# Optimization experiments

Hardware: AMD Instinct MI355X
Metric: run time of the kernel (lower is better)

## Reference

```python
import jax, jax.numpy as jnp
import numpy as np

B, R, C, NC = 8, 1000, 1024, 81
H, W = 1024, 1024
MEANS = jnp.array([0.0, 0.0, 0.0, 0.0], jnp.float32)
STDS = jnp.array([0.1, 0.1, 0.2, 0.2], jnp.float32)
MIN_CONF = 0.05
NMS_THR = 0.5
MAX_INST = 100
NEG = -1e9


def setup_inputs() -> dict:
    key = jax.random.key(0)
    k1, k2, k3, k4, k5 = jax.random.split(key, 5)
    x = jax.random.normal(k1, (B * R, C), jnp.float32)
    w_cls = jax.random.normal(k2, (C, NC), jnp.float32) * 0.01
    b_cls = jnp.zeros((NC,), jnp.float32)
    w_delta = jax.random.normal(k3, (C, 4), jnp.float32) * 0.01
    b_delta = jnp.zeros((4,), jnp.float32)
    # rois: (batch_ind, y1, x1, y2, x2), normalized coords with y1<y2, x1<x2
    yx1 = jax.random.uniform(k4, (B * R, 2), jnp.float32) * 0.7
    hw = jax.random.uniform(k5, (B * R, 2), jnp.float32) * 0.28 + 0.02
    bind = jnp.repeat(jnp.arange(B, dtype=jnp.float32), R)[:, None]
    rois = jnp.concatenate([bind, yx1, yx1 + hw], axis=1)
    return {"x": x, "w_cls": w_cls, "b_cls": b_cls, "w_delta": w_delta, "b_delta": b_delta, "rois": rois}


def delta2bbox(rois, deltas):
    # rois, deltas: [N, 4] in (y1, x1, y2, x2) / (dy, dx, dh, dw)
    d = deltas * STDS + MEANS
    h = rois[:, 2] - rois[:, 0]
    w = rois[:, 3] - rois[:, 1]
    cy = rois[:, 0] + 0.5 * h + d[:, 0] * h
    cx = rois[:, 1] + 0.5 * w + d[:, 1] * w
    h = h * jnp.exp(d[:, 2])
    w = w * jnp.exp(d[:, 3])
    return jnp.stack([cy - 0.5 * h, cx - 0.5 * w, cy + 0.5 * h, cx + 0.5 * w], axis=1)


def pairwise_iou(boxes):
    # boxes: [N, 4]
    area = (boxes[:, 2] - boxes[:, 0]) * (boxes[:, 3] - boxes[:, 1])
    y1 = jnp.maximum(boxes[:, None, 0], boxes[None, :, 0])
    x1 = jnp.maximum(boxes[:, None, 1], boxes[None, :, 1])
    y2 = jnp.minimum(boxes[:, None, 2], boxes[None, :, 2])
    x2 = jnp.minimum(boxes[:, None, 3], boxes[None, :, 3])
    inter = jnp.maximum(y2 - y1, 0.0) * jnp.maximum(x2 - x1, 0.0)
    union = area[:, None] + area[None, :] - inter
    return inter / jnp.maximum(union, 1e-8)


def nms_single(boxes, scores, class_ids, valid):
    # boxes [R,4], scores [R], class_ids [R] int, valid [R] bool -> detections [MAX_INST, 6]
    masked = jnp.where(valid, scores, NEG)
    order = jnp.argsort(-masked)  # descending score
    b = boxes[order]
    s = masked[order]
    c = class_ids[order]
    v = valid[order]
    # class-aware IoU: cross-class pairs never suppress each other
    iou = pairwise_iou(b) * (c[:, None] == c[None, :]).astype(boxes.dtype)
    n = b.shape[0]

    def step(supp, xs):
        i, iou_row, vi = xs
        keep_i = vi & ~supp[i]
        supp = supp | jnp.where(keep_i, iou_row > NMS_THR, False)
        return supp, keep_i

    _, keep = jax.lax.scan(step, jnp.zeros((n,), bool), (jnp.arange(n), iou, v))
    final = jnp.where(keep, s, NEG)
    top_s, top_i = jax.lax.top_k(final, MAX_INST)
    ok = (top_s > NEG / 2)[:, None]
    det = jnp.concatenate([b[top_i], c[top_i].astype(boxes.dtype)[:, None], s[top_i][:, None]], axis=1)
    return jnp.where(ok, det, 0.0)


def reference(x, w_cls, b_cls, w_delta, b_delta, rois):
    logits = x @ w_cls + b_cls                      # [B*R, NC]
    probs = jax.nn.softmax(logits, axis=-1)
    deltas = x @ w_delta + b_delta                  # [B*R, 4]

    probs_b = probs.reshape(B, R, NC)
    class_ids = jnp.argmax(probs_b, axis=-1).astype(jnp.int32)           # [B, R]
    class_scores = jnp.take_along_axis(probs_b, class_ids[..., None], axis=-1)[..., 0]

    scale = jnp.array([H, W, H, W], jnp.float32)
    boxes = rois[:, 1:5] * scale                    # pixel coords, [B*R, 4]
    refined = delta2bbox(boxes, deltas)
    window = jnp.array([0.0, 0.0, float(H), float(W)], jnp.float32)
    refined = jnp.clip(refined, window[jnp.array([0, 1, 0, 1])], window[jnp.array([2, 3, 2, 3])])
    refined = refined.reshape(B, R, 4)

    valid = (class_ids > 0) & (class_scores >= MIN_CONF)
    detections = jax.vmap(nms_single)(refined, class_scores, class_ids, valid)  # [B, MAX_INST, 6]
    return detections
```

## Files before the change

### kernel.cpp

```cpp
#include <hip/hip_runtime.h>
#include <math.h>
#include <stdint.h>

#define RR 1000
#define CC 1024
#define NCLS 81
#define HH 1024.0f
#define MIN_CONF_V 0.05f
#define NMS_THR_V 0.5f
#define NEGV -1e9f

typedef __attribute__((ext_vector_type(8))) short bf16x8;
typedef __attribute__((ext_vector_type(4))) float f32x4;

__device__ __forceinline__ unsigned short f2bf(float f) {
    unsigned int u = __float_as_uint(f);
    return (unsigned short)((u + 0x7FFFu + ((u >> 16) & 1u)) >> 16);
}
__device__ __forceinline__ float bf2f(unsigned short h) {
    return __uint_as_float(((unsigned int)h) << 16);
}

__global__ __launch_bounds__(64) void k0_pack(
    const float* __restrict__ w_cls, const float* __restrict__ w_delta,
    unsigned short* __restrict__ wh, unsigned short* __restrict__ wl)
{
    const int ct = blockIdx.x >> 5;
    const int sg = blockIdx.x & 31;
    const int l = threadIdx.x;
    const int col = ct * 16 + (l & 15);
    const int kbase = sg * 32 + (l >> 4) * 8;
    unsigned short h[8], lo[8];
    #pragma unroll
    for (int j = 0; j < 8; ++j) {
        const int k = kbase + j;
        float v = 0.f;
        if (col < NCLS)          v = w_cls[(size_t)k * NCLS + col];
        else if (col < NCLS + 4) v = w_delta[(size_t)k * 4 + (col - NCLS)];
        h[j] = f2bf(v);
        lo[j] = f2bf(v - bf2f(h[j]));
    }
    const size_t base = ((size_t)(ct * 32 + sg) * 64 + l) * 8;
    uint4 uh, ul;
    uh.x = (unsigned)h[0] | ((unsigned)h[1] << 16);
    uh.y = (unsigned)h[2] | ((unsigned)h[3] << 16);
    uh.z = (unsigned)h[4] | ((unsigned)h[5] << 16);
    uh.w = (unsigned)h[6] | ((unsigned)h[7] << 16);
    ul.x = (unsigned)lo[0] | ((unsigned)lo[1] << 16);
    ul.y = (unsigned)lo[2] | ((unsigned)lo[3] << 16);
    ul.z = (unsigned)lo[4] | ((unsigned)lo[5] << 16);
    ul.w = (unsigned)lo[6] | ((unsigned)lo[7] << 16);
    *(uint4*)&wh[base] = uh;
    *(uint4*)&wl[base] = ul;
}

__global__ __launch_bounds__(384) void k1_head(
    const float* __restrict__ x,
    const unsigned short* __restrict__ wh, const unsigned short* __restrict__ wl,
    const float* __restrict__ b_cls, const float* __restrict__ b_delta,
    const float* __restrict__ rois,
    float* __restrict__ bx_ws, float* __restrict__ sc_ws, float* __restrict__ cid_ws)
{
    __shared__ __align__(16) unsigned short xh[2][16][64];
    __shared__ __align__(16) unsigned short xl[2][16][64];
    __shared__ float outb[16 * 104];

    const int t = threadIdx.x;
    const int lane = t & 63;
    const int ct = t >> 6;
    const int row0 = blockIdx.x * 16;

    const int srow = t >> 4;
    const int sk4 = (t & 15) * 4;
    const size_t xsrc = (size_t)(row0 + srow) * CC + sk4;

    const int aoff0 = (lane & 15) * 64 + ((lane >> 4) << 3);
    const int aoff1 = aoff0 + 32;

    const unsigned short* whp = wh + ((size_t)(ct * 32) * 64 + lane) * 8;
    const unsigned short* wlp = wl + ((size_t)(ct * 32) * 64 + lane) * 8;
    const size_t bstep = 64 * 8;

    f32x4 acc = {0.f, 0.f, 0.f, 0.f};

    float4 xv = make_float4(0.f, 0.f, 0.f, 0.f);
    if (t < 256) xv = *(const float4*)(x + xsrc);

    bf16x8 B0h = *(const bf16x8*)(whp + 0 * bstep);
    bf16x8 B0l = *(const bf16x8*)(wlp + 0 * bstep);
    bf16x8 B1h = *(const bf16x8*)(whp + 1 * bstep);
    bf16x8 B1l = *(const bf16x8*)(wlp + 1 * bstep);

    int cur = 0;
    for (int c = 0; c < 16; ++c) {
        if (t < 256) {
            unsigned short h0 = f2bf(xv.x), h1 = f2bf(xv.y), h2 = f2bf(xv.z), h3 = f2bf(xv.w);
            ushort4 hv = make_ushort4(h0, h1, h2, h3);
            ushort4 lv = make_ushort4(f2bf(xv.x - bf2f(h0)), f2bf(xv.y - bf2f(h1)),
                                      f2bf(xv.z - bf2f(h2)), f2bf(xv.w - bf2f(h3)));
            *(ushort4*)&xh[cur][srow][sk4] = hv;
            *(ushort4*)&xl[cur][srow][sk4] = lv;
        }
        __syncthreads();

        bf16x8 N0h, N0l, N1h, N1l;
        if (c < 15) {
            if (t < 256) xv = *(const float4*)(x + xsrc + (size_t)(c + 1) * 64);
            const size_t sg = (size_t)(2 * c + 2);
            N0h = *(const bf16x8*)(whp + sg * bstep);
            N0l = *(const bf16x8*)(wlp + sg * bstep);
            N1h = *(const bf16x8*)(whp + (sg + 1) * bstep);
            N1l = *(const bf16x8*)(wlp + (sg + 1) * bstep);
        }

        const bf16x8 a0h = *(const bf16x8*)&((const unsigned short*)xh[cur])[aoff0];
        const bf16x8 a0l = *(const bf16x8*)&((const unsigned short*)xl[cur])[aoff0];
        acc = __builtin_amdgcn_mfma_f32_16x16x32_bf16(a0h, B0h, acc, 0, 0, 0);
        acc = __builtin_amdgcn_mfma_f32_16x16x32_bf16(a0h, B0l, acc, 0, 0, 0);
        acc = __builtin_amdgcn_mfma_f32_16x16x32_bf16(a0l, B0h, acc, 0, 0, 0);
        const bf16x8 a1h = *(const bf16x8*)&((const unsigned short*)xh[cur])[aoff1];
        const bf16x8 a1l = *(const bf16x8*)&((const unsigned short*)xl[cur])[aoff1];
        acc = __builtin_amdgcn_mfma_f32_16x16x32_bf16(a1h, B1h, acc, 0, 0, 0);
        acc = __builtin_amdgcn_mfma_f32_16x16x32_bf16(a1h, B1l, acc, 0, 0, 0);
        acc = __builtin_amdgcn_mfma_f32_16x16x32_bf16(a1l, B1h, acc, 0, 0, 0);

        B0h = N0h; B0l = N0l; B1h = N1h; B1l = N1l;
        cur ^= 1;
        __syncthreads();
    }

    #pragma unroll
    for (int r = 0; r < 4; ++r)
        outb[((lane >> 4) * 4 + r) * 104 + ct * 16 + (lane & 15)] = acc[r];
    __syncthreads();

    if (t < 256) {
        const int row = t >> 4;
        const int e = t & 15;
        float vmax = -INFINITY;
        int imax = 1 << 20;
        float v[6];
        #pragma unroll
        for (int s = 0; s < 6; ++s) {
            const int cidx = e + 16 * s;
            if (cidx < NCLS) {
                const float val = outb[row * 104 + cidx] + b_cls[cidx];
                v[s] = val;
                if (val > vmax) { vmax = val; imax = cidx; }
            } else v[s] = -INFINITY;
        }
        #pragma unroll
        for (int m = 8; m >= 1; m >>= 1) {
            const float v2 = __shfl_xor(vmax, m);
            const int   i2 = __shfl_xor(imax, m);
            if (v2 > vmax || (v2 == vmax && i2 < imax)) { vmax = v2; imax = i2; }
        }
        float sume = 0.f;
        #pragma unroll
        for (int s = 0; s < 6; ++s) {
            const int cidx = e + 16 * s;
            if (cidx < NCLS) sume += expf(v[s] - vmax);
        }
        #pragma unroll
        for (int m = 8; m >= 1; m >>= 1) sume += __shfl_xor(sume, m);

        if (e == 0) {
            const int gr = row0 + row;
            const float score = 1.0f / sume;
            const int cid = imax;
            const float d0 = (outb[row * 104 + 81] + b_delta[0]) * 0.1f;
            const float d1 = (outb[row * 104 + 82] + b_delta[1]) * 0.1f;
            const float d2 = (outb[row * 104 + 83] + b_delta[2]) * 0.2f;
            const float d3 = (outb[row * 104 + 84] + b_delta[3]) * 0.2f;
            const float y1 = rois[(size_t)gr * 5 + 1] * HH;
            const float x1 = rois[(size_t)gr * 5 + 2] * HH;
            const float y2 = rois[(size_t)gr * 5 + 3] * HH;
            const float x2 = rois[(size_t)gr * 5 + 4] * HH;
            const float h = y2 - y1, w = x2 - x1;
            const float cy = y1 + 0.5f * h + d0 * h;
            const float cx = x1 + 0.5f * w + d1 * w;
            const float h2 = h * expf(d2);
            const float w2 = w * expf(d3);
            const float by1 = fminf(fmaxf(cy - 0.5f * h2, 0.f), HH);
            const float bx1 = fminf(fmaxf(cx - 0.5f * w2, 0.f), HH);
            const float by2 = fminf(fmaxf(cy + 0.5f * h2, 0.f), HH);
            const float bx2 = fminf(fmaxf(cx + 0.5f * w2, 0.f), HH);
            const bool valid = (cid > 0) && (score >= MIN_CONF_V);
            bx_ws[(size_t)gr * 4 + 0] = by1;
            bx_ws[(size_t)gr * 4 + 1] = bx1;
            bx_ws[(size_t)gr * 4 + 2] = by2;
            bx_ws[(size_t)gr * 4 + 3] = bx2;
            sc_ws[gr]  = valid ? score : NEGV;
            cid_ws[gr] = (float)cid;
        }
    }
}

__global__ __launch_bounds__(256) void k2_nms(
    const float* __restrict__ bx_ws, const float* __restrict__ sc_ws,
    const float* __restrict__ cid_ws, float* __restrict__ det)
{
    __shared__ unsigned long long keys[256];
    __shared__ float sy1[256], sx1[256], sy2[256], sx2[256];
    __shared__ float scl[256], ssc[256];
    __shared__ unsigned char supp[256];
    __shared__ int s_cnt, s_num;

    const int b = blockIdx.x;
    const int t = threadIdx.x;
    const int base = b * RR;

    keys[t] = 0ull;
    if (t == 0) { s_cnt = 0; s_num = 0; }
    __syncthreads();

    for (int r = t; r < RR; r += 256) {
        const float s = sc_ws[base + r];
        if (s > NEGV * 0.5f) {
            const int i = atomicAdd(&s_num, 1);
            if (i < 256) {
                unsigned int u = __float_as_uint(s) | 0x80000000u;
                keys[i] = ((unsigned long long)u << 32) | (unsigned int)(~(unsigned int)r);
            }
        }
    }
    __syncthreads();
    const int V = (s_num < 256) ? s_num : 256;

    for (int k = 2; k <= 256; k <<= 1) {
        for (int j = k >> 1; j > 0; j >>= 1) {
            const int ixj = t ^ j;
            if (ixj > t) {
                const unsigned long long a = keys[t];
                const unsigned long long c = keys[ixj];
                const bool desc = ((t & k) == 0);
                if (desc ? (a < c) : (a > c)) { keys[t] = c; keys[ixj] = a; }
            }
            __syncthreads();
        }
    }

    if (t < V) {
        const int orig = (int)(~(unsigned int)keys[t]);
        const int g = base + orig;
        sy1[t] = bx_ws[(size_t)g * 4 + 0];
        sx1[t] = bx_ws[(size_t)g * 4 + 1];
        sy2[t] = bx_ws[(size_t)g * 4 + 2];
        sx2[t] = bx_ws[(size_t)g * 4 + 3];
        scl[t] = cid_ws[g];
        ssc[t] = sc_ws[g];
    } else {
        sy1[t] = sx1[t] = sy2[t] = sx2[t] = 0.f;
        scl[t] = -1.f;
        ssc[t] = NEGV;
    }
    supp[t] = 0;
    __syncthreads();

    for (int i = 0; i < V; ++i) {
        __syncthreads();
        if (s_cnt >= 100) break;
        if (!supp[i]) {
            if (t > i && t < V && scl[t] == scl[i]) {
                const float yy1 = fmaxf(sy1[i], sy1[t]);
                const float xx1 = fmaxf(sx1[i], sx1[t]);
                const float yy2 = fminf(sy2[i], sy2[t]);
                const float xx2 = fminf(sx2[i], sx2[t]);
                const float inter = fmaxf(yy2 - yy1, 0.f) * fmaxf(xx2 - xx1, 0.f);
                const float ai = (sy2[i] - sy1[i]) * (sx2[i] - sx1[i]);
                const float at = (sy2[t] - sy1[t]) * (sx2[t] - sx1[t]);
                const float uni = ai + at - inter;
                if (inter / fmaxf(uni, 1e-8f) > NMS_THR_V) supp[t] = 1;
            }
            if (t == 0) {
                const int slot = s_cnt;
                if (slot < 100) {
                    float* o = det + ((size_t)b * 100 + slot) * 6;
                    o[0] = sy1[i]; o[1] = sx1[i]; o[2] = sy2[i]; o[3] = sx2[i];
                    o[4] = scl[i]; o[5] = ssc[i];
                }
                s_cnt = slot + 1;
            }
        }
    }
    __syncthreads();
    int cnt = s_cnt;
    if (cnt > 100) cnt = 100;
    for (int idx = t; idx < 600; idx += 256) {
        if (idx >= cnt * 6) det[(size_t)b * 600 + idx] = 0.f;
    }
}

extern "C" void kernel_launch(void* const* d_in, const int* in_sizes, int n_in,
                              void* d_out, int out_size, void* d_ws, size_t ws_size,
                              hipStream_t stream) {
    const float* x       = (const float*)d_in[0];
    const float* w_cls   = (const float*)d_in[1];
    const float* b_cls   = (const float*)d_in[2];
    const float* w_delta = (const float*)d_in[3];
    const float* b_delta = (const float*)d_in[4];
    const float* rois    = (const float*)d_in[5];
    float* out = (float*)d_out;

    float* bx_ws   = (float*)d_ws;
    float* sc_ws   = bx_ws + 8000 * 4;
    float* cid_ws  = sc_ws + 8000;
    unsigned short* wh = (unsigned short*)(cid_ws + 8000);
    unsigned short* wl = wh + 98304;

    k0_pack<<<192, 64, 0, stream>>>(w_cls, w_delta, wh, wl);
    k1_head<<<500, 384, 0, stream>>>(x, wh, wl, b_cls, b_delta, rois,
                                     bx_ws, sc_ws, cid_ws);
    k2_nms<<<8, 256, 0, stream>>>(bx_ws, sc_ws, cid_ws, out);
}
```

Before: 32.99 us.

## Process 32 rows per head block and swizzle LDS to cut bank conflicts

The head GEMM block now covers 32 ROI rows instead of 16, so each wave runs two MFMA accumulator chains that share the same weight fragments. This halves the weight loads from global memory and halves the grid to 250 blocks. LDS staging of x uses an XOR swizzle on the column index to avoid bank conflicts on the fragment reads. The softmax epilogue is remapped to 8 lanes per row. In exchange there are fewer blocks than CUs to spread over, and per-thread work and register use go up.

Result: no change. 33.14 us (+0.4%).

```diff
diff --git a/kernel.cpp b/kernel.cpp
--- a/kernel.cpp
+++ b/kernel.cpp
@@ -61,30 +61,41 @@
     const float* __restrict__ rois,
     float* __restrict__ bx_ws, float* __restrict__ sc_ws, float* __restrict__ cid_ws)
 {
-    __shared__ __align__(16) unsigned short xh[2][16][64];
-    __shared__ __align__(16) unsigned short xl[2][16][64];
-    __shared__ float outb[16 * 104];
+    __shared__ __align__(16) unsigned short xh[2][32][64];
+    __shared__ __align__(16) unsigned short xl[2][32][64];
+    __shared__ float outb[32 * 104];
 
     const int t = threadIdx.x;
     const int lane = t & 63;
     const int ct = t >> 6;
-    const int row0 = blockIdx.x * 16;
-
-    const int srow = t >> 4;
-    const int sk4 = (t & 15) * 4;
-    const size_t xsrc = (size_t)(row0 + srow) * CC + sk4;
-
-    const int aoff0 = (lane & 15) * 64 + ((lane >> 4) << 3);
-    const int aoff1 = aoff0 + 32;
+    const int row0 = blockIdx.x * 32;
+
+    const int srow0 = t >> 4;
+    const int sc4 = t & 15;
+    const int sd0 = (sc4 ^ ((srow0 & 7) << 1)) * 4;
+    const size_t xsrc0 = (size_t)(row0 + srow0) * CC + sc4 * 4;
+    const int srow1 = 24 + (t >> 4);
+    const int sd1 = (sc4 ^ ((srow1 & 7) << 1)) * 4;
+    const size_t xsrc1 = (size_t)(row0 + srow1) * CC + sc4 * 4;
+
+    const int r = lane & 15;
+    const int m = lane >> 4;
+    const int e2 = (r & 7) << 1;
+    const int a00 = r * 64        + (((m << 1) + 0) ^ e2) * 4;
+    const int a01 = r * 64        + (((m << 1) + 8) ^ e2) * 4;
+    const int a10 = (r + 16) * 64 + (((m << 1) + 0) ^ e2) * 4;
+    const int a11 = (r + 16) * 64 + (((m << 1) + 8) ^ e2) * 4;
 
     const unsigned short* whp = wh + ((size_t)(ct * 32) * 64 + lane) * 8;
     const unsigned short* wlp = wl + ((size_t)(ct * 32) * 64 + lane) * 8;
     const size_t bstep = 64 * 8;
 
-    f32x4 acc = {0.f, 0.f, 0.f, 0.f};
-
-    float4 xv = make_float4(0.f, 0.f, 0.f, 0.f);
-    if (t < 256) xv = *(const float4*)(x + xsrc);
+    f32x4 acc0 = {0.f, 0.f, 0.f, 0.f};
+    f32x4 acc1 = {0.f, 0.f, 0.f, 0.f};
+
+    float4 xv0 = *(const float4*)(x + xsrc0);
+    float4 xv1 = make_float4(0.f, 0.f, 0.f, 0.f);
+    if (t < 128) xv1 = *(const float4*)(x + xsrc1);
 
     bf16x8 B0h = *(const bf16x8*)(whp + 0 * bstep);
     bf16x8 B0l = *(const bf16x8*)(wlp + 0 * bstep);
@@ -93,19 +104,27 @@
 
     int cur = 0;
     for (int c = 0; c < 16; ++c) {
-        if (t < 256) {
-            unsigned short h0 = f2bf(xv.x), h1 = f2bf(xv.y), h2 = f2bf(xv.z), h3 = f2bf(xv.w);
-            ushort4 hv = make_ushort4(h0, h1, h2, h3);
-            ushort4 lv = make_ushort4(f2bf(xv.x - bf2f(h0)), f2bf(xv.y - bf2f(h1)),
-                                      f2bf(xv.z - bf2f(h2)), f2bf(xv.w - bf2f(h3)));
-            *(ushort4*)&xh[cur][srow][sk4] = hv;
-            *(ushort4*)&xl[cur][srow][sk4] = lv;
+        {
+            unsigned short h0 = f2bf(xv0.x), h1 = f2bf(xv0.y), h2 = f2bf(xv0.z), h3 = f2bf(xv0.w);
+            *(ushort4*)&xh[cur][srow0][sd0] = make_ushort4(h0, h1, h2, h3);
+            *(ushort4*)&xl[cur][srow0][sd0] = make_ushort4(
+                f2bf(xv0.x - bf2f(h0)), f2bf(xv0.y - bf2f(h1)),
+                f2bf(xv0.z - bf2f(h2)), f2bf(xv0.w - bf2f(h3)));
+            if (t < 128) {
+                unsigned short g0 = f2bf(xv1.x), g1 = f2bf(xv1.y), g2 = f2bf(xv1.z), g3 = f2bf(xv1.w);
+                *(ushort4*)&xh[cur][srow1][sd1] = make_ushort4(g0, g1, g2, g3);
+                *(ushort4*)&xl[cur][srow1][sd1] = make_ushort4(
+                    f2bf(xv1.x - bf2f(g0)), f2bf(xv1.y - bf2f(g1)),
+                    f2bf(xv1.z - bf2f(g2)), f2bf(xv1.w - bf2f(g3)));
+            }
         }
         __syncthreads();
 
-        bf16x8 N0h, N0l, N1h, N1l;
+        bf16x8 N0h = B0h, N0l = B0l, N1h = B1h, N1l = B1l;
         if (c < 15) {
-            if (t < 256) xv = *(const float4*)(x + xsrc + (size_t)(c + 1) * 64);
+            const size_t off = (size_t)(c + 1) * 64;
+            xv0 = *(const float4*)(x + xsrc0 + off);
+            if (t < 128) xv1 = *(const float4*)(x + xsrc1 + off);
             const size_t sg = (size_t)(2 * c + 2);
             N0h = *(const bf16x8*)(whp + sg * bstep);
             N0l = *(const bf16x8*)(wlp + sg * bstep);
@@ -113,16 +132,28 @@
             N1l = *(const bf16x8*)(wlp + (sg + 1) * bstep);
         }
 
-        const bf16x8 a0h = *(const bf16x8*)&((const unsigned short*)xh[cur])[aoff0];
-        const bf16x8 a0l = *(const bf16x8*)&((const unsigned short*)xl[cur])[aoff0];
-        acc = __builtin_amdgcn_mfma_f32_16x16x32_bf16(a0h, B0h, acc, 0, 0, 0);
-        acc = __builtin_amdgcn_mfma_f32_16x16x32_bf16(a0h, B0l, acc, 0, 0, 0);
-        acc = __builtin_amdgcn_mfma_f32_16x16x32_bf16(a0l, B0h, acc, 0, 0, 0);
-        const bf16x8 a1h = *(const bf16x8*)&((const unsigned short*)xh[cur])[aoff1];
-        const bf16x8 a1l = *(const bf16x8*)&((const unsigned short*)xl[cur])[aoff1];
-        acc = __builtin_amdgcn_mfma_f32_16x16x32_bf16(a1h, B1h, acc, 0, 0, 0);
-        acc = __builtin_amdgcn_mfma_f32_16x16x32_bf16(a1h, B1l, acc, 0, 0, 0);
-        acc = __builtin_amdgcn_mfma_f32_16x16x32_bf16(a1l, B1h, acc, 0, 0, 0);
+        const unsigned short* hb = (const unsigned short*)xh[cur];
+        const unsigned short* lb = (const unsigned short*)xl[cur];
+        const bf16x8 a0h = *(const bf16x8*)(hb + a00);
+        const bf16x8 a0l = *(const bf16x8*)(lb + a00);
+        const bf16x8 a2h = *(const bf16x8*)(hb + a10);
+        const bf16x8 a2l = *(const bf16x8*)(lb + a10);
+        acc0 = __builtin_amdgcn_mfma_f32_16x16x32_bf16(a0h, B0h, acc0, 0, 0, 0);
+        acc1 = __builtin_amdgcn_mfma_f32_16x16x32_bf16(a2h, B0h, acc1, 0, 0, 0);
+        acc0 = __builtin_amdgcn_mfma_f32_16x16x32_bf16(a0h, B0l, acc0, 0, 0, 0);
+        acc1 = __builtin_amdgcn_mfma_f32_16x16x32_bf16(a2h, B0l, acc1, 0, 0, 0);
+        acc0 = __builtin_amdgcn_mfma_f32_16x16x32_bf16(a0l, B0h, acc0, 0, 0, 0);
+        acc1 = __builtin_amdgcn_mfma_f32_16x16x32_bf16(a2l, B0h, acc1, 0, 0, 0);
+        const bf16x8 a1h = *(const bf16x8*)(hb + a01);
+        const bf16x8 a1l = *(const bf16x8*)(lb + a01);
+        const bf16x8 a3h = *(const bf16x8*)(hb + a11);
+        const bf16x8 a3l = *(const bf16x8*)(lb + a11);
+        acc0 = __builtin_amdgcn_mfma_f32_16x16x32_bf16(a1h, B1h, acc0, 0, 0, 0);
+        acc1 = __builtin_amdgcn_mfma_f32_16x16x32_bf16(a3h, B1h, acc1, 0, 0, 0);
+        acc0 = __builtin_amdgcn_mfma_f32_16x16x32_bf16(a1h, B1l, acc0, 0, 0, 0);
+        acc1 = __builtin_amdgcn_mfma_f32_16x16x32_bf16(a3h, B1l, acc1, 0, 0, 0);
+        acc0 = __builtin_amdgcn_mfma_f32_16x16x32_bf16(a1l, B1h, acc0, 0, 0, 0);
+        acc1 = __builtin_amdgcn_mfma_f32_16x16x32_bf16(a3l, B1h, acc1, 0, 0, 0);
 
         B0h = N0h; B0l = N0l; B1h = N1h; B1l = N1l;
         cur ^= 1;
@@ -130,19 +161,21 @@
     }
 
     #pragma unroll
-    for (int r = 0; r < 4; ++r)
-        outb[((lane >> 4) * 4 + r) * 104 + ct * 16 + (lane & 15)] = acc[r];
+    for (int rr = 0; rr < 4; ++rr) {
+        outb[((lane >> 4) * 4 + rr) * 104 + ct * 16 + (lane & 15)] = acc0[rr];
+        outb[((lane >> 4) * 4 + rr + 16) * 104 + ct * 16 + (lane & 15)] = acc1[rr];
+    }
     __syncthreads();
 
     if (t < 256) {
-        const int row = t >> 4;
-        const int e = t & 15;
+        const int row = t >> 3;
+        const int e = t & 7;
         float vmax = -INFINITY;
         int imax = 1 << 20;
-        float v[6];
+        float v[12];
         #pragma unroll
-        for (int s = 0; s < 6; ++s) {
-            const int cidx = e + 16 * s;
+        for (int s = 0; s < 12; ++s) {
+            const int cidx = e + 8 * s;
             if (cidx < NCLS) {
                 const float val = outb[row * 104 + cidx] + b_cls[cidx];
                 v[s] = val;
@@ -150,19 +183,19 @@
             } else v[s] = -INFINITY;
         }
         #pragma unroll
-        for (int m = 8; m >= 1; m >>= 1) {
-            const float v2 = __shfl_xor(vmax, m);
-            const int   i2 = __shfl_xor(imax, m);
+        for (int mm = 4; mm >= 1; mm >>= 1) {
+            const float v2 = __shfl_xor(vmax, mm);
+            const int   i2 = __shfl_xor(imax, mm);
             if (v2 > vmax || (v2 == vmax && i2 < imax)) { vmax = v2; imax = i2; }
         }
         float sume = 0.f;
         #pragma unroll
-        for (int s = 0; s < 6; ++s) {
-            const int cidx = e + 16 * s;
+        for (int s = 0; s < 12; ++s) {
+            const int cidx = e + 8 * s;
             if (cidx < NCLS) sume += expf(v[s] - vmax);
         }
         #pragma unroll
-        for (int m = 8; m >= 1; m >>= 1) sume += __shfl_xor(sume, m);
+        for (int mm = 4; mm >= 1; mm >>= 1) sume += __shfl_xor(sume, mm);
 
         if (e == 0) {
             const int gr = row0 + row;
@@ -309,7 +342,7 @@
     unsigned short* wl = wh + 98304;
 
     k0_pack<<<192, 64, 0, stream>>>(w_cls, w_delta, wh, wl);
-    k1_head<<<500, 384, 0, stream>>>(x, wh, wl, b_cls, b_delta, rois,
+    k1_head<<<250, 384, 0, stream>>>(x, wh, wl, b_cls, b_delta, rois,
                                      bx_ws, sc_ws, cid_ws);
     k2_nms<<<8, 256, 0, stream>>>(bx_ws, sc_ws, cid_ws, out);
 }
```

## Use 32x32 MFMA tiles with split-K waves and full-tile LDS staging

Applied to the files above, without the earlier changes.

The head GEMM now processes 32 rows per block using 32x32x16 bf16 MFMA. The two waves per column tile split K in half, and their partial sums are added during the softmax epilogue. Weight packing is reorganised for the new operand layout. The whole 32x1024 x tile is converted to hi/lo bf16 and staged in padded LDS up front, which replaces the double-buffered per-chunk loop. The goal is fewer sync points and better MFMA efficiency. The cost is a large LDS footprint (about 133KB, one block per CU), only 250 blocks, and no overlap between loading x and the matmul.

Result: faster. 30.70 us (-7.0%).

```diff
diff --git a/kernel.cpp b/kernel.cpp
--- a/kernel.cpp
+++ b/kernel.cpp
@@ -10,8 +10,10 @@
 #define NMS_THR_V 0.5f
 #define NEGV -1e9f
 
+#define KSTRIDE 520
+
 typedef __attribute__((ext_vector_type(8))) short bf16x8;
-typedef __attribute__((ext_vector_type(4))) float f32x4;
+typedef __attribute__((ext_vector_type(16))) float f32x16;
 
 __device__ __forceinline__ unsigned short f2bf(float f) {
     unsigned int u = __float_as_uint(f);
@@ -25,11 +27,11 @@
     const float* __restrict__ w_cls, const float* __restrict__ w_delta,
     unsigned short* __restrict__ wh, unsigned short* __restrict__ wl)
 {
-    const int ct = blockIdx.x >> 5;
-    const int sg = blockIdx.x & 31;
+    const int ct = blockIdx.x >> 6;
+    const int ks = blockIdx.x & 63;
     const int l = threadIdx.x;
-    const int col = ct * 16 + (l & 15);
-    const int kbase = sg * 32 + (l >> 4) * 8;
+    const int col = ct * 32 + (l & 31);
+    const int kbase = ks * 16 + (l >> 5) * 8;
     unsigned short h[8], lo[8];
     #pragma unroll
     for (int j = 0; j < 8; ++j) {
@@ -40,7 +42,7 @@
         h[j] = f2bf(v);
         lo[j] = f2bf(v - bf2f(h[j]));
     }
-    const size_t base = ((size_t)(ct * 32 + sg) * 64 + l) * 8;
+    const size_t base = ((size_t)(ct * 64 + ks) * 64 + l) * 8;
     uint4 uh, ul;
     uh.x = (unsigned)h[0] | ((unsigned)h[1] << 16);
     uh.y = (unsigned)h[2] | ((unsigned)h[3] << 16);
@@ -61,117 +63,127 @@
     const float* __restrict__ rois,
     float* __restrict__ bx_ws, float* __restrict__ sc_ws, float* __restrict__ cid_ws)
 {
-    __shared__ __align__(16) unsigned short xh[2][16][64];
-    __shared__ __align__(16) unsigned short xl[2][16][64];
-    __shared__ float outb[16 * 104];
+    __shared__ __align__(16) unsigned short XH[64 * KSTRIDE];
+    __shared__ __align__(16) unsigned short XL[64 * KSTRIDE];
 
     const int t = threadIdx.x;
     const int lane = t & 63;
-    const int ct = t >> 6;
-    const int row0 = blockIdx.x * 16;
-
-    const int srow = t >> 4;
-    const int sk4 = (t & 15) * 4;
-    const size_t xsrc = (size_t)(row0 + srow) * CC + sk4;
-
-    const int aoff0 = (lane & 15) * 64 + ((lane >> 4) << 3);
-    const int aoff1 = aoff0 + 32;
-
-    const unsigned short* whp = wh + ((size_t)(ct * 32) * 64 + lane) * 8;
-    const unsigned short* wlp = wl + ((size_t)(ct * 32) * 64 + lane) * 8;
-    const size_t bstep = 64 * 8;
-
-    f32x4 acc = {0.f, 0.f, 0.f, 0.f};
-
-    float4 xv = make_float4(0.f, 0.f, 0.f, 0.f);
-    if (t < 256) xv = *(const float4*)(x + xsrc);
-
-    bf16x8 B0h = *(const bf16x8*)(whp + 0 * bstep);
-    bf16x8 B0l = *(const bf16x8*)(wlp + 0 * bstep);
-    bf16x8 B1h = *(const bf16x8*)(whp + 1 * bstep);
-    bf16x8 B1l = *(const bf16x8*)(wlp + 1 * bstep);
-
-    int cur = 0;
-    for (int c = 0; c < 16; ++c) {
-        if (t < 256) {
-            unsigned short h0 = f2bf(xv.x), h1 = f2bf(xv.y), h2 = f2bf(xv.z), h3 = f2bf(xv.w);
-            ushort4 hv = make_ushort4(h0, h1, h2, h3);
-            ushort4 lv = make_ushort4(f2bf(xv.x - bf2f(h0)), f2bf(xv.y - bf2f(h1)),
-                                      f2bf(xv.z - bf2f(h2)), f2bf(xv.w - bf2f(h3)));
-            *(ushort4*)&xh[cur][srow][sk4] = hv;
-            *(ushort4*)&xl[cur][srow][sk4] = lv;
-        }
-        __syncthreads();
-
-        bf16x8 N0h, N0l, N1h, N1l;
-        if (c < 15) {
-            if (t < 256) xv = *(const float4*)(x + xsrc + (size_t)(c + 1) * 64);
-            const size_t sg = (size_t)(2 * c + 2);
-            N0h = *(const bf16x8*)(whp + sg * bstep);
-            N0l = *(const bf16x8*)(wlp + sg * bstep);
-            N1h = *(const bf16x8*)(whp + (sg + 1) * bstep);
-            N1l = *(const bf16x8*)(wlp + (sg + 1) * bstep);
-        }
-
-        const bf16x8 a0h = *(const bf16x8*)&((const unsigned short*)xh[cur])[aoff0];
-        const bf16x8 a0l = *(const bf16x8*)&((const unsigned short*)xl[cur])[aoff0];
-        acc = __builtin_amdgcn_mfma_f32_16x16x32_bf16(a0h, B0h, acc, 0, 0, 0);
-        acc = __builtin_amdgcn_mfma_f32_16x16x32_bf16(a0h, B0l, acc, 0, 0, 0);
-        acc = __builtin_amdgcn_mfma_f32_16x16x32_bf16(a0l, B0h, acc, 0, 0, 0);
-        const bf16x8 a1h = *(const bf16x8*)&((const unsigned short*)xh[cur])[aoff1];
-        const bf16x8 a1l = *(const bf16x8*)&((const unsigned short*)xl[cur])[aoff1];
-        acc = __builtin_amdgcn_mfma_f32_16x16x32_bf16(a1h, B1h, acc, 0, 0, 0);
-        acc = __builtin_amdgcn_mfma_f32_16x16x32_bf16(a1h, B1l, acc, 0, 0, 0);
-        acc = __builtin_amdgcn_mfma_f32_16x16x32_bf16(a1l, B1h, acc, 0, 0, 0);
-
-        B0h = N0h; B0l = N0l; B1h = N1h; B1l = N1l;
-        cur ^= 1;
-        __syncthreads();
-    }
-
-    #pragma unroll
-    for (int r = 0; r < 4; ++r)
-        outb[((lane >> 4) * 4 + r) * 104 + ct * 16 + (lane & 15)] = acc[r];
+    const int wid = t >> 6;
+    const int ct = wid >> 1;
+    const int half = wid & 1;
+    const int row0 = blockIdx.x * 32;
+
+    #pragma unroll
+    for (int batch = 0; batch < 2; ++batch) {
+        float4 v[11];
+        #pragma unroll
+        for (int i = 0; i < 11; ++i) {
+            const int s = t + (batch * 11 + i) * 384;
+            if (s < 8192)
+                v[i] = *(const float4*)(x + (size_t)(row0 + (s >> 8)) * CC + (s & 255) * 4);
+        }
+        #pragma unroll
+        for (int i = 0; i < 11; ++i) {
+            const int s = t + (batch * 11 + i) * 384;
+            if (s < 8192) {
+                const int row = s >> 8;
+                const int f4 = s & 255;
+                const int ks = f4 >> 2;
+                const int q = f4 & 3;
+                const int lane_ = ((q >> 1) << 5) + row;
+                const int j0 = (q & 1) * 4;
+                const size_t us = (size_t)ks * KSTRIDE + lane_ * 8 + j0;
+                const unsigned short h0 = f2bf(v[i].x), h1 = f2bf(v[i].y),
+                                     h2 = f2bf(v[i].z), h3 = f2bf(v[i].w);
+                *(ushort4*)&XH[us] = make_ushort4(h0, h1, h2, h3);
+                *(ushort4*)&XL[us] = make_ushort4(
+                    f2bf(v[i].x - bf2f(h0)), f2bf(v[i].y - bf2f(h1)),
+                    f2bf(v[i].z - bf2f(h2)), f2bf(v[i].w - bf2f(h3)));
+            }
+        }
+    }
+    __syncthreads();
+
+    const int ks0 = half * 32;
+    const unsigned short* whp = wh + (((size_t)ct * 64 + ks0) * 64 + lane) * 8;
+    const unsigned short* wlp = wl + (((size_t)ct * 64 + ks0) * 64 + lane) * 8;
+    const unsigned short* ap  = &XH[(size_t)ks0 * KSTRIDE + lane * 8];
+    const unsigned short* alp = &XL[(size_t)ks0 * KSTRIDE + lane * 8];
+
+    f32x16 acc = {0.f,0.f,0.f,0.f,0.f,0.f,0.f,0.f,0.f,0.f,0.f,0.f,0.f,0.f,0.f,0.f};
+
+    bf16x8 BH[4], BL[4];
+    #pragma unroll
+    for (int i = 0; i < 4; ++i) {
+        BH[i] = *(const bf16x8*)(whp + (size_t)i * 512);
+        BL[i] = *(const bf16x8*)(wlp + (size_t)i * 512);
+    }
+
+    #pragma unroll
+    for (int ks = 0; ks < 32; ++ks) {
+        const bf16x8 bh = BH[ks & 3];
+        const bf16x8 bl = BL[ks & 3];
+        if (ks + 4 < 32) {
+            BH[ks & 3] = *(const bf16x8*)(whp + (size_t)(ks + 4) * 512);
+            BL[ks & 3] = *(const bf16x8*)(wlp + (size_t)(ks + 4) * 512);
+        }
+        const bf16x8 ah = *(const bf16x8*)(ap  + (size_t)ks * KSTRIDE);
+        const bf16x8 al = *(const bf16x8*)(alp + (size_t)ks * KSTRIDE);
+        acc = __builtin_amdgcn_mfma_f32_32x32x16_bf16(ah, bh, acc, 0, 0, 0);
+        acc = __builtin_amdgcn_mfma_f32_32x32x16_bf16(ah, bl, acc, 0, 0, 0);
+        acc = __builtin_amdgcn_mfma_f32_32x32x16_bf16(al, bh, acc, 0, 0, 0);
+    }
+    __syncthreads();
+
+    float* outH = (float*)XH;
+    float* outT = outH + 3200;
+    float* dst = half ? outT : outH;
+    const int col = lane & 31;
+    #pragma unroll
+    for (int reg = 0; reg < 16; ++reg) {
+        const int row = (reg & 3) + 8 * (reg >> 2) + 4 * (lane >> 5);
+        dst[row * 100 + ct * 32 + col] = acc[reg];
+    }
     __syncthreads();
 
     if (t < 256) {
-        const int row = t >> 4;
-        const int e = t & 15;
+        const int row = t >> 3;
+        const int e = t & 7;
         float vmax = -INFINITY;
         int imax = 1 << 20;
-        float v[6];
-        #pragma unroll
-        for (int s = 0; s < 6; ++s) {
-            const int cidx = e + 16 * s;
+        float vv[12];
+        #pragma unroll
+        for (int s = 0; s < 12; ++s) {
+            const int cidx = e + 8 * s;
             if (cidx < NCLS) {
-                const float val = outb[row * 104 + cidx] + b_cls[cidx];
-                v[s] = val;
+                const float val = outH[row * 100 + cidx] + outT[row * 100 + cidx] + b_cls[cidx];
+                vv[s] = val;
                 if (val > vmax) { vmax = val; imax = cidx; }
-            } else v[s] = -INFINITY;
-        }
-        #pragma unroll
-        for (int m = 8; m >= 1; m >>= 1) {
-            const float v2 = __shfl_xor(vmax, m);
-            const int   i2 = __shfl_xor(imax, m);
+            } else vv[s] = -INFINITY;
+        }
+        #pragma unroll
+        for (int mm = 4; mm >= 1; mm >>= 1) {
+            const float v2 = __shfl_xor(vmax, mm);
+            const int   i2 = __shfl_xor(imax, mm);
             if (v2 > vmax || (v2 == vmax && i2 < imax)) { vmax = v2; imax = i2; }
         }
         float sume = 0.f;
         #pragma unroll
-        for (int s = 0; s < 6; ++s) {
-            const int cidx = e + 16 * s;
-            if (cidx < NCLS) sume += expf(v[s] - vmax);
-        }
-        #pragma unroll
-        for (int m = 8; m >= 1; m >>= 1) sume += __shfl_xor(sume, m);
+        for (int s = 0; s < 12; ++s) {
+            const int cidx = e + 8 * s;
+            if (cidx < NCLS) sume += expf(vv[s] - vmax);
+        }
+        #pragma unroll
+        for (int mm = 4; mm >= 1; mm >>= 1) sume += __shfl_xor(sume, mm);
 
         if (e == 0) {
             const int gr = row0 + row;
             const float score = 1.0f / sume;
             const int cid = imax;
-            const float d0 = (outb[row * 104 + 81] + b_delta[0]) * 0.1f;
-            const float d1 = (outb[row * 104 + 82] + b_delta[1]) * 0.1f;
-            const float d2 = (outb[row * 104 + 83] + b_delta[2]) * 0.2f;
-            const float d3 = (outb[row * 104 + 84] + b_delta[3]) * 0.2f;
+            const float d0 = (outH[row * 100 + 81] + outT[row * 100 + 81] + b_delta[0]) * 0.1f;
+            const float d1 = (outH[row * 100 + 82] + outT[row * 100 + 82] + b_delta[1]) * 0.1f;
+            const float d2 = (outH[row * 100 + 83] + outT[row * 100 + 83] + b_delta[2]) * 0.2f;
+            const float d3 = (outH[row * 100 + 84] + outT[row * 100 + 84] + b_delta[3]) * 0.2f;
             const float y1 = rois[(size_t)gr * 5 + 1] * HH;
             const float x1 = rois[(size_t)gr * 5 + 2] * HH;
             const float y2 = rois[(size_t)gr * 5 + 3] * HH;
@@ -214,13 +226,13 @@
     if (t == 0) { s_cnt = 0; s_num = 0; }
     __syncthreads();
 
-    for (int r = t; r < RR; r += 256) {
-        const float s = sc_ws[base + r];
+    for (int rr = t; rr < RR; rr += 256) {
+        const float s = sc_ws[base + rr];
         if (s > NEGV * 0.5f) {
             const int i = atomicAdd(&s_num, 1);
             if (i < 256) {
                 unsigned int u = __float_as_uint(s) | 0x80000000u;
-                keys[i] = ((unsigned long long)u << 32) | (unsigned int)(~(unsigned int)r);
+                keys[i] = ((unsigned long long)u << 32) | (unsigned int)(~(unsigned int)rr);
             }
         }
     }
@@ -309,7 +321,7 @@
     unsigned short* wl = wh + 98304;
 
     k0_pack<<<192, 64, 0, stream>>>(w_cls, w_delta, wh, wl);
-    k1_head<<<500, 384, 0, stream>>>(x, wh, wl, b_cls, b_delta, rois,
+    k1_head<<<250, 384, 0, stream>>>(x, wh, wl, b_cls, b_delta, rois,
                                      bx_ws, sc_ws, cid_ws);
     k2_nms<<<8, 256, 0, stream>>>(bx_ws, sc_ws, cid_ws, out);
 }
```
